# Performance work log

Measured on AMD Instinct MI355X. Metric: run time of the kernel, lower is better.

Reference implementation:

```python
import jax, jax.numpy as jnp
import numpy as np

B, Q, V, H = 8, 128, 512, 512


def setup_inputs() -> dict:
    key = jax.random.key(0)
    ks = jax.random.split(key, 6)
    s = 1.0 / np.sqrt(H)
    return {
        "query": jax.random.normal(ks[0], (B, Q, H), jnp.float32),
        "values": jax.random.normal(ks[1], (B, V, H), jnp.float32),
        "mask": jax.random.randint(ks[2], (B, V), 0, 2, jnp.int32),
        "Wq": jax.random.normal(ks[3], (H, H), jnp.float32) * s,
        "bq": jnp.zeros((H,), jnp.float32),
        "Wv": jax.random.normal(ks[4], (H, H), jnp.float32) * s,
        "bv": jnp.zeros((H,), jnp.float32),
        "wc": jax.random.normal(ks[5], (H, 1), jnp.float32) * s,
        "bc": jnp.zeros((1,), jnp.float32),
    }


def reference(query, values, mask, Wq, bq, Wv, bv, wc, bc):
    # Project once per token (Q*H and V*H GEMMs), then broadcast-add:
    # faithful to tanh(Lq(q)[:, :, None] + Lv(v)[:, None]) since Linear is
    # applied along the last dim and broadcasting commutes with it.
    qp = jnp.einsum('bqh,kh->bqk', query, Wq) + bq          # [B,Q,H]
    vp = jnp.einsum('bvh,kh->bvk', values, Wv) + bv          # [B,V,H]
    added = jnp.tanh(qp[:, :, None, :] + vp[:, None, :, :])  # [B,Q,V,H]
    scores = jnp.einsum('bqvh,ho->bqv', added, wc) + bc[0]   # [B,Q,V]
    neg_inf = jnp.array(-jnp.inf, scores.dtype)
    scores = jnp.where(mask[:, None, :] == 0, neg_inf, scores)
    weights = jax.nn.softmax(scores, axis=-1)                # [B,Q,V]
    context = jnp.einsum('bqv,bvh->bqh', weights, values)    # [B,Q,H]
    return (context, weights)
```

## Files before the change

kernel.cpp:

```cpp
#include <hip/hip_runtime.h>
#include <hip/hip_bf16.h>


#define C_SCALE 2.8853900817779268f

typedef __attribute__((ext_vector_type(8))) short short8;
typedef __attribute__((ext_vector_type(4))) float f32x4;

__device__ __forceinline__ float fexp2(float x) { return __builtin_amdgcn_exp2f(x); }
__device__ __forceinline__ float frcp(float x)  { return __builtin_amdgcn_rcpf(x); }

__device__ __forceinline__ void bf_split(float x, short& hi, short& lo) {
  unsigned u = __builtin_bit_cast(unsigned, x);
  unsigned r = u + 0x7fffu + ((u >> 16) & 1u);
  hi = (short)(r >> 16);
  float hf = __builtin_bit_cast(float, r & 0xffff0000u);
  lo = (short)(__builtin_bit_cast(unsigned, x - hf) >> 16);
}

__global__ __launch_bounds__(256) void proj_gemm_mfma(
    const float* __restrict__ query, const float* __restrict__ values,
    const float* __restrict__ Wq, const float* __restrict__ Wv,
    const float* __restrict__ bq, const float* __restrict__ bv,
    float* __restrict__ qp, float* __restrict__ vp)
{
  __shared__ short sAhi[64 * 72];
  __shared__ short sAlo[64 * 72];
  __shared__ short sWhi[64 * 72];
  __shared__ short sWlo[64 * 72];

  const int t    = threadIdx.x;
  const int lane = t & 63;
  const int w    = t >> 6;
  const int by   = blockIdx.y;
  const bool isQ = (by < 16);
  const float* A    = isQ ? query : values;
  const float* W    = isQ ? Wq : Wv;
  const float* bias = isQ ? bq : bv;
  float*       out  = isQ ? qp : vp;
  const int m0 = (isQ ? by : (by - 16)) << 6;
  const int n0 = blockIdx.x << 6;

  const int srow = t >> 2, scol = t & 3;
  const float* Ap = A + (size_t)(m0 + srow) * 512 + (scol << 2);
  const float* Wp = W + (size_t)(n0 + srow) * 512 + (scol << 2);

  const int mw = (w & 1) << 5, nw = (w >> 1) << 5;
  const int frow = lane & 15, fquad = lane >> 4;

  f32x4 acc[2][2] = {};
  float4 pfA[4], pfW[4];
#pragma unroll
  for (int p = 0; p < 4; ++p) {
    pfA[p] = *(const float4*)(Ap + (p << 4));
    pfW[p] = *(const float4*)(Wp + (p << 4));
  }

  for (int kc = 0; kc < 512; kc += 64) {
    __syncthreads();
#pragma unroll
    for (int p = 0; p < 4; ++p) {
      float av[4] = {pfA[p].x, pfA[p].y, pfA[p].z, pfA[p].w};
      float wv[4] = {pfW[p].x, pfW[p].y, pfW[p].z, pfW[p].w};
      short4 ah, al, wh, wl;
      short* ahp = (short*)&ah; short* alp = (short*)&al;
      short* whp = (short*)&wh; short* wlp = (short*)&wl;
#pragma unroll
      for (int k = 0; k < 4; ++k) {
        bf_split(av[k], ahp[k], alp[k]);
        bf_split(wv[k], whp[k], wlp[k]);
      }
      const int ofs = srow * 72 + ((p << 2) + scol) * 4;
      *(short4*)&sAhi[ofs] = ah; *(short4*)&sAlo[ofs] = al;
      *(short4*)&sWhi[ofs] = wh; *(short4*)&sWlo[ofs] = wl;
    }
    __syncthreads();
    if (kc + 64 < 512) {
#pragma unroll
      for (int p = 0; p < 4; ++p) {
        pfA[p] = *(const float4*)(Ap + kc + 64 + (p << 4));
        pfW[p] = *(const float4*)(Wp + kc + 64 + (p << 4));
      }
    }
#pragma unroll
    for (int kb = 0; kb < 2; ++kb) {
      const int ko = kb * 32 + fquad * 8;
      short8 ahi[2], alo[2], whi[2], wlo[2];
#pragma unroll
      for (int mt = 0; mt < 2; ++mt) {
        const int r = (mw + mt * 16 + frow) * 72 + ko;
        ahi[mt] = *(const short8*)&sAhi[r];
        alo[mt] = *(const short8*)&sAlo[r];
      }
#pragma unroll
      for (int nt = 0; nt < 2; ++nt) {
        const int r = (nw + nt * 16 + frow) * 72 + ko;
        whi[nt] = *(const short8*)&sWhi[r];
        wlo[nt] = *(const short8*)&sWlo[r];
      }
#pragma unroll
      for (int mt = 0; mt < 2; ++mt)
#pragma unroll
        for (int nt = 0; nt < 2; ++nt) {
          acc[mt][nt] = __builtin_amdgcn_mfma_f32_16x16x32_bf16(
              alo[mt], whi[nt], acc[mt][nt], 0, 0, 0);
          acc[mt][nt] = __builtin_amdgcn_mfma_f32_16x16x32_bf16(
              ahi[mt], wlo[nt], acc[mt][nt], 0, 0, 0);
          acc[mt][nt] = __builtin_amdgcn_mfma_f32_16x16x32_bf16(
              ahi[mt], whi[nt], acc[mt][nt], 0, 0, 0);
        }
    }
  }

#pragma unroll
  for (int nt = 0; nt < 2; ++nt) {
    const int n = n0 + nw + nt * 16 + frow;
    const float bn = bias[n];
#pragma unroll
    for (int mt = 0; mt < 2; ++mt) {
      float vreg[4] = {acc[mt][nt].x, acc[mt][nt].y, acc[mt][nt].z, acc[mt][nt].w};
#pragma unroll
      for (int r = 0; r < 4; ++r) {
        const int m = m0 + mw + mt * 16 + fquad * 4 + r;
        out[(size_t)m * 512 + n] = vreg[r] + bn;
      }
    }
  }
}

template<int NU>
__device__ __forceinline__ void score_chunk(
    const float* __restrict__ vpb, const float* __restrict__ qr0,
    const float* __restrict__ qr1, const float* __restrict__ wc,
    const int* idxs, float* wls0, float* wls1,
    int sbase, int i0, int g, int c4, int cnt, int lane)
{
  unsigned voff[NU];
  float a0[NU], a1[NU];
#pragma unroll
  for (int u = 0; u < NU; ++u) {
    const int s = (sbase + ((i0 + u) << 2) + g) & 511;
    voff[u] = ((unsigned)idxs[s] << 9) + (unsigned)c4;
    a0[u] = 0.f; a1[u] = 0.f;
  }
#pragma unroll
  for (int j = 0; j < 8; ++j) {
    const int hoff = (j << 6) + c4;
    const float4 q0v = *(const float4*)(qr0 + hoff);
    const float4 q1v = *(const float4*)(qr1 + hoff);
    const float4 wcv = *(const float4*)(wc + hoff);
    const unsigned jo = (unsigned)(j << 6);
    float4 vv[NU];
#pragma unroll
    for (int u = 0; u < NU; ++u)
      vv[u] = *(const float4*)(vpb + (voff[u] + jo));
    const float cq0[4] = {C_SCALE * q0v.x, C_SCALE * q0v.y,
                          C_SCALE * q0v.z, C_SCALE * q0v.w};
    const float dd[4]  = {fexp2(C_SCALE * (q1v.x - q0v.x)),
                          fexp2(C_SCALE * (q1v.y - q0v.y)),
                          fexp2(C_SCALE * (q1v.z - q0v.z)),
                          fexp2(C_SCALE * (q1v.w - q0v.w))};
    const float wc4[4] = {wcv.x, wcv.y, wcv.z, wcv.w};
#pragma unroll
    for (int u = 0; u < NU; ++u) {
      const float vq[4] = {vv[u].x, vv[u].y, vv[u].z, vv[u].w};
#pragma unroll
      for (int k = 0; k < 4; ++k) {
        float x0 = __builtin_fmaf(C_SCALE, vq[k], cq0[k]);
        float e0 = fexp2(x0);
        float e1 = e0 * dd[k];
        float d0 = e0 + 1.0f;
        float d1 = e1 + 1.0f;
        float P  = frcp(d0 * d1);
        a0[u] = __builtin_fmaf(wc4[k] * d1, P, a0[u]);
        a1[u] = __builtin_fmaf(wc4[k] * d0, P, a1[u]);
      }
    }
  }
#pragma unroll
  for (int u = 0; u < NU; ++u) {
    const int i = i0 + u;
    float s0 = a0[u], s1 = a1[u];
#pragma unroll
    for (int off = 1; off < 16; off <<= 1) {
      s0 += __shfl_xor(s0, off, 64);
      s1 += __shfl_xor(s1, off, 64);
    }
    const int s = sbase + (i << 2) + g;
    if ((lane & 15) == i && s < cnt) { wls0[s] = s0; wls1[s] = s1; }
  }
}

__global__ __launch_bounds__(512) void attn_fused(
    const float* __restrict__ qp, const float* __restrict__ vp,
    const float* __restrict__ values, const int* __restrict__ mask,
    const float* __restrict__ wc,
    float* __restrict__ out_ctx, float* __restrict__ out_w)
{
  __shared__ int   idxs[512];
  __shared__ float wls[2][512];
  __shared__ float wls2[512][2];
  __shared__ int   cnt8[8];

  const int t    = threadIdx.x;
  const int lane = t & 63;
  const int w    = t >> 6;
  const int b    = blockIdx.x & 7;
  const int qg   = blockIdx.x >> 3;
  const int rowbase = b * 128 + qg * 2;

  ((float*)wls)[t]        = 3.4e38f;
  ((float*)wls)[t + 512]  = 3.4e38f;
  ((float*)wls2)[t]       = 0.f;
  ((float*)wls2)[t + 512] = 0.f;
  idxs[t] = 0;
  if (t < 256) {
    float4 z = {0.f, 0.f, 0.f, 0.f};
    ((float4*)(out_w + (size_t)rowbase * 512))[t] = z;
  }
  const int mv = mask[b * 512 + t];
  const unsigned long long bal = __ballot(mv != 0);
  if (lane == 0) cnt8[w] = __popcll(bal);
  __syncthreads();
  int cnt = 0, offw = 0;
#pragma unroll
  for (int j = 0; j < 8; ++j) { if (j == w) offw = cnt; cnt += cnt8[j]; }
  if (mv) {
    int rank = __popcll(bal & ((1ull << lane) - 1ull));
    idxs[offw + rank] = t;
  }
  __syncthreads();

  const int NSTEP = (cnt + 31) >> 5;
  const int sbase = w * (NSTEP << 2);
  const int g  = lane >> 4;
  const int c4 = (lane & 15) << 2;

  const float* vpb = vp + (size_t)b * 512 * 512;
  const float* qr0 = qp + (size_t)rowbase * 512;
  const float* qr1 = qr0 + 512;

  int i0 = 0;
  for (; i0 + 4 <= NSTEP; i0 += 4)
    score_chunk<4>(vpb, qr0, qr1, wc, idxs, wls[0], wls[1],
                   sbase, i0, g, c4, cnt, lane);
  for (; i0 < NSTEP; ++i0)
    score_chunk<1>(vpb, qr0, qr1, wc, idxs, wls[0], wls[1],
                   sbase, i0, g, c4, cnt, lane);
  __syncthreads();

  {
    const int mq = (w >= 4) ? 1 : 0;
    const float* sc = wls[mq];
    float4 u0 = ((const float4*)sc)[lane * 2];
    float4 u1 = ((const float4*)sc)[lane * 2 + 1];
    float s8[8] = {u0.x, u0.y, u0.z, u0.w, u1.x, u1.y, u1.z, u1.w};
    float m = s8[0];
#pragma unroll
    for (int k = 1; k < 8; ++k) m = fminf(m, s8[k]);
#pragma unroll
    for (int off = 1; off < 64; off <<= 1) m = fminf(m, __shfl_xor(m, off, 64));
    float e[8], S = 0.f;
#pragma unroll
    for (int k = 0; k < 8; ++k) { e[k] = fexp2(C_SCALE * (m - s8[k])); S += e[k]; }
#pragma unroll
    for (int off = 1; off < 64; off <<= 1) S += __shfl_xor(S, off, 64);
    const float rinv = frcp(S);
    if (w == 0 || w == 4) {
      float* owq = out_w + (size_t)(rowbase + mq) * 512;
#pragma unroll
      for (int k = 0; k < 8; ++k) {
        const int s = lane * 8 + k;
        const float wgt = e[k] * rinv;
        wls2[s][mq] = wgt;
        if (s < cnt) owq[idxs[s]] = wgt;
      }
    }
  }
  __syncthreads();

  const int NC = (cnt + 3) >> 2;
  const unsigned hbase = (unsigned)(w * 64 + c4);
  const float* vb = values + (size_t)b * 512 * 512;
  float c0[4] = {0.f, 0.f, 0.f, 0.f}, c1[4] = {0.f, 0.f, 0.f, 0.f};
#pragma unroll 4
  for (int i = 0; i < NC; ++i) {
    const int s = (i << 2) + g;
    const unsigned ro = ((unsigned)idxs[s] << 9) + hbase;
    const float2 wg = *(const float2*)&wls2[s][0];
    const float4 v4 = *(const float4*)(vb + ro);
    float vv[4] = {v4.x, v4.y, v4.z, v4.w};
#pragma unroll
    for (int k = 0; k < 4; ++k) {
      c0[k] = __builtin_fmaf(wg.x, vv[k], c0[k]);
      c1[k] = __builtin_fmaf(wg.y, vv[k], c1[k]);
    }
  }
#pragma unroll
  for (int k = 0; k < 4; ++k) {
    c0[k] += __shfl_xor(c0[k], 16, 64); c0[k] += __shfl_xor(c0[k], 32, 64);
    c1[k] += __shfl_xor(c1[k], 16, 64); c1[k] += __shfl_xor(c1[k], 32, 64);
  }
  if (lane < 16) {
    float4 o0 = {c0[0], c0[1], c0[2], c0[3]};
    float4 o1 = {c1[0], c1[1], c1[2], c1[3]};
    *(float4*)(out_ctx + (size_t)rowbase * 512 + w * 64 + lane * 4)       = o0;
    *(float4*)(out_ctx + (size_t)(rowbase + 1) * 512 + w * 64 + lane * 4) = o1;
  }
}

extern "C" void kernel_launch(void* const* d_in, const int* in_sizes, int n_in,
                              void* d_out, int out_size, void* d_ws, size_t ws_size,
                              hipStream_t stream) {
  const float* query  = (const float*)d_in[0];
  const float* values = (const float*)d_in[1];
  const int*   mask   = (const int*)d_in[2];
  const float* Wq     = (const float*)d_in[3];
  const float* bq     = (const float*)d_in[4];
  const float* Wv     = (const float*)d_in[5];
  const float* bv     = (const float*)d_in[6];
  const float* wc     = (const float*)d_in[7];

  float* out = (float*)d_out;
  float* qp  = (float*)d_ws;
  float* vp  = qp + (size_t)1024 * 512;

  proj_gemm_mfma<<<dim3(8, 80), 256, 0, stream>>>(query, values, Wq, Wv, bq, bv, qp, vp);
  attn_fused<<<512, 512, 0, stream>>>(qp, vp, values, mask, wc,
                                      out, out + (size_t)8 * 128 * 512);
}
```

Before: 145.8 us.

## Split fused attention into score and finish kernels with 4-way key split

Splits the fused attention kernel into a score kernel launched on a 512x4 grid of 256-thread blocks, each handling a quarter of the unmasked keys. Scores are staged in the weights output buffer instead of shared memory, and a second kernel runs softmax, scatters the weights and computes the context. The goal is more concurrent blocks and better latency hiding for the dominant tanh-score work. In exchange it adds a kernel launch, recomputes the mask compaction in each block, and round-trips the scores through global memory.

```diff
diff --git a/kernel.cpp b/kernel.cpp
--- a/kernel.cpp
+++ b/kernel.cpp
@@ -129,31 +129,30 @@
 }
 
 template<int NU>
-__device__ __forceinline__ void score_chunk(
+__device__ __forceinline__ void score_chunkA(
     const float* __restrict__ vpb, const float* __restrict__ qr0,
-    const float* __restrict__ qr1, const float* __restrict__ wc,
-    const int* idxs, float* wls0, float* wls1,
-    int sbase, int i0, int g, int c4, int cnt, int lane)
+    const float* __restrict__ wc, const int* idxs, float* __restrict__ ow0,
+    int s00, int i0, int hi, int c4, int lane)
 {
+  int su[NU];
   unsigned voff[NU];
   float a0[NU], a1[NU];
 #pragma unroll
   for (int u = 0; u < NU; ++u) {
-    const int s = (sbase + ((i0 + u) << 2) + g) & 511;
-    voff[u] = ((unsigned)idxs[s] << 9) + (unsigned)c4;
+    su[u] = s00 + ((i0 + u) << 4);
+    voff[u] = ((unsigned)idxs[su[u] & 511] << 9) + (unsigned)c4;
     a0[u] = 0.f; a1[u] = 0.f;
   }
 #pragma unroll
   for (int j = 0; j < 8; ++j) {
     const int hoff = (j << 6) + c4;
+    float4 vv[NU];
+#pragma unroll
+    for (int u = 0; u < NU; ++u)
+      vv[u] = *(const float4*)(vpb + voff[u] + (unsigned)(j << 6));
     const float4 q0v = *(const float4*)(qr0 + hoff);
-    const float4 q1v = *(const float4*)(qr1 + hoff);
+    const float4 q1v = *(const float4*)(qr0 + 512 + hoff);
     const float4 wcv = *(const float4*)(wc + hoff);
-    const unsigned jo = (unsigned)(j << 6);
-    float4 vv[NU];
-#pragma unroll
-    for (int u = 0; u < NU; ++u)
-      vv[u] = *(const float4*)(vpb + (voff[u] + jo));
     const float cq0[4] = {C_SCALE * q0v.x, C_SCALE * q0v.y,
                           C_SCALE * q0v.z, C_SCALE * q0v.w};
     const float dd[4]  = {fexp2(C_SCALE * (q1v.x - q0v.x)),
@@ -179,28 +178,26 @@
   }
 #pragma unroll
   for (int u = 0; u < NU; ++u) {
-    const int i = i0 + u;
     float s0 = a0[u], s1 = a1[u];
 #pragma unroll
     for (int off = 1; off < 16; off <<= 1) {
       s0 += __shfl_xor(s0, off, 64);
       s1 += __shfl_xor(s1, off, 64);
     }
-    const int s = sbase + (i << 2) + g;
-    if ((lane & 15) == i && s < cnt) { wls0[s] = s0; wls1[s] = s1; }
-  }
-}
-
-__global__ __launch_bounds__(512) void attn_fused(
+    if (su[u] < hi && (lane & 15) == (i0 + u)) {
+      ow0[su[u]]       = s0;
+      ow0[512 + su[u]] = s1;
+    }
+  }
+}
+
+__global__ __launch_bounds__(256, 8) void attn_score(
     const float* __restrict__ qp, const float* __restrict__ vp,
-    const float* __restrict__ values, const int* __restrict__ mask,
-    const float* __restrict__ wc,
-    float* __restrict__ out_ctx, float* __restrict__ out_w)
+    const int* __restrict__ mask, const float* __restrict__ wc,
+    float* __restrict__ out_w)
 {
-  __shared__ int   idxs[512];
-  __shared__ float wls[2][512];
-  __shared__ float wls2[512][2];
-  __shared__ int   cnt8[8];
+  __shared__ int idxs[512];
+  __shared__ int cnt8[8];
 
   const int t    = threadIdx.x;
   const int lane = t & 63;
@@ -209,15 +206,61 @@
   const int qg   = blockIdx.x >> 3;
   const int rowbase = b * 128 + qg * 2;
 
-  ((float*)wls)[t]        = 3.4e38f;
-  ((float*)wls)[t + 512]  = 3.4e38f;
+  idxs[t] = 0; idxs[t + 256] = 0;
+  const int mv0 = mask[b * 512 + t];
+  const int mv1 = mask[b * 512 + 256 + t];
+  const unsigned long long bal0 = __ballot(mv0 != 0);
+  const unsigned long long bal1 = __ballot(mv1 != 0);
+  if (lane == 0) { cnt8[w] = __popcll(bal0); cnt8[w + 4] = __popcll(bal1); }
+  __syncthreads();
+  int cnt = 0, off0 = 0, off4 = 0;
+#pragma unroll
+  for (int j = 0; j < 8; ++j) {
+    if (j == w)     off0 = cnt;
+    if (j == w + 4) off4 = cnt;
+    cnt += cnt8[j];
+  }
+  if (mv0) idxs[off0 + __popcll(bal0 & ((1ull << lane) - 1ull))] = t;
+  if (mv1) idxs[off4 + __popcll(bal1 & ((1ull << lane) - 1ull))] = t + 256;
+  __syncthreads();
+
+  const int c  = blockIdx.y;
+  const int lo = (cnt * c) >> 2;
+  const int hi = (cnt * (c + 1)) >> 2;
+  const int NI = (hi - lo + 15) >> 4;
+  const int g  = lane >> 4;
+  const int c4 = (lane & 15) << 2;
+  const int s00 = lo + (w << 2) + g;
+
+  const float* vpb = vp + (size_t)b * 512 * 512;
+  const float* qr0 = qp + (size_t)rowbase * 512;
+  float* ow0 = out_w + (size_t)rowbase * 512;
+
+  int i0 = 0;
+  for (; i0 + 2 <= NI; i0 += 2)
+    score_chunkA<2>(vpb, qr0, wc, idxs, ow0, s00, i0, hi, c4, lane);
+  for (; i0 < NI; ++i0)
+    score_chunkA<1>(vpb, qr0, wc, idxs, ow0, s00, i0, hi, c4, lane);
+}
+
+__global__ __launch_bounds__(512) void attn_finish(
+    const float* __restrict__ values, const int* __restrict__ mask,
+    float* __restrict__ out_ctx, float* __restrict__ out_w)
+{
+  __shared__ int   idxs[512];
+  __shared__ float wls2[512][2];
+  __shared__ int   cnt8[8];
+
+  const int t    = threadIdx.x;
+  const int lane = t & 63;
+  const int w    = t >> 6;
+  const int b    = blockIdx.x & 7;
+  const int qg   = blockIdx.x >> 3;
+  const int rowbase = b * 128 + qg * 2;
+
   ((float*)wls2)[t]       = 0.f;
   ((float*)wls2)[t + 512] = 0.f;
   idxs[t] = 0;
-  if (t < 256) {
-    float4 z = {0.f, 0.f, 0.f, 0.f};
-    ((float4*)(out_w + (size_t)rowbase * 512))[t] = z;
-  }
   const int mv = mask[b * 512 + t];
   const unsigned long long bal = __ballot(mv != 0);
   if (lane == 0) cnt8[w] = __popcll(bal);
@@ -225,36 +268,22 @@
   int cnt = 0, offw = 0;
 #pragma unroll
   for (int j = 0; j < 8; ++j) { if (j == w) offw = cnt; cnt += cnt8[j]; }
+  int iinv = -1;
   if (mv) {
-    int rank = __popcll(bal & ((1ull << lane) - 1ull));
-    idxs[offw + rank] = t;
-  }
-  __syncthreads();
-
-  const int NSTEP = (cnt + 31) >> 5;
-  const int sbase = w * (NSTEP << 2);
-  const int g  = lane >> 4;
-  const int c4 = (lane & 15) << 2;
-
-  const float* vpb = vp + (size_t)b * 512 * 512;
-  const float* qr0 = qp + (size_t)rowbase * 512;
-  const float* qr1 = qr0 + 512;
-
-  int i0 = 0;
-  for (; i0 + 4 <= NSTEP; i0 += 4)
-    score_chunk<4>(vpb, qr0, qr1, wc, idxs, wls[0], wls[1],
-                   sbase, i0, g, c4, cnt, lane);
-  for (; i0 < NSTEP; ++i0)
-    score_chunk<1>(vpb, qr0, qr1, wc, idxs, wls[0], wls[1],
-                   sbase, i0, g, c4, cnt, lane);
+    iinv = offw + __popcll(bal & ((1ull << lane) - 1ull));
+    idxs[iinv] = t;
+  }
   __syncthreads();
 
   {
     const int mq = (w >= 4) ? 1 : 0;
-    const float* sc = wls[mq];
-    float4 u0 = ((const float4*)sc)[lane * 2];
-    float4 u1 = ((const float4*)sc)[lane * 2 + 1];
+    const float* srow = out_w + (size_t)(rowbase + mq) * 512;
+    float4 u0 = ((const float4*)srow)[lane * 2];
+    float4 u1 = ((const float4*)srow)[lane * 2 + 1];
     float s8[8] = {u0.x, u0.y, u0.z, u0.w, u1.x, u1.y, u1.z, u1.w};
+#pragma unroll
+    for (int k = 0; k < 8; ++k)
+      if (lane * 8 + k >= cnt) s8[k] = 3.4e38f;
     float m = s8[0];
 #pragma unroll
     for (int k = 1; k < 8; ++k) m = fminf(m, s8[k]);
@@ -267,19 +296,25 @@
     for (int off = 1; off < 64; off <<= 1) S += __shfl_xor(S, off, 64);
     const float rinv = frcp(S);
     if (w == 0 || w == 4) {
-      float* owq = out_w + (size_t)(rowbase + mq) * 512;
 #pragma unroll
       for (int k = 0; k < 8; ++k) {
         const int s = lane * 8 + k;
-        const float wgt = e[k] * rinv;
-        wls2[s][mq] = wgt;
-        if (s < cnt) owq[idxs[s]] = wgt;
-      }
-    }
-  }
-  __syncthreads();
+        if (s < cnt) wls2[s][mq] = e[k] * rinv;
+      }
+    }
+  }
+  __syncthreads();
+
+  {
+    float w0 = 0.f, w1 = 0.f;
+    if (iinv >= 0) { w0 = wls2[iinv][0]; w1 = wls2[iinv][1]; }
+    out_w[(size_t)rowbase * 512 + t]       = w0;
+    out_w[(size_t)(rowbase + 1) * 512 + t] = w1;
+  }
 
   const int NC = (cnt + 3) >> 2;
+  const int g  = lane >> 4;
+  const int c4 = (lane & 15) << 2;
   const unsigned hbase = (unsigned)(w * 64 + c4);
   const float* vb = values + (size_t)b * 512 * 512;
   float c0[4] = {0.f, 0.f, 0.f, 0.f}, c1[4] = {0.f, 0.f, 0.f, 0.f};
@@ -321,11 +356,12 @@
   const float* bv     = (const float*)d_in[6];
   const float* wc     = (const float*)d_in[7];
 
-  float* out = (float*)d_out;
-  float* qp  = (float*)d_ws;
-  float* vp  = qp + (size_t)1024 * 512;
+  float* out   = (float*)d_out;
+  float* out_w = out + (size_t)8 * 128 * 512;
+  float* qp    = (float*)d_ws;
+  float* vp    = qp + (size_t)1024 * 512;
 
   proj_gemm_mfma<<<dim3(8, 80), 256, 0, stream>>>(query, values, Wq, Wv, bq, bv, qp, vp);
-  attn_fused<<<512, 512, 0, stream>>>(qp, vp, values, mask, wc,
-                                      out, out + (size_t)8 * 128 * 512);
-}
+  attn_score<<<dim3(512, 4), 256, 0, stream>>>(qp, vp, mask, wc, out_w);
+  attn_finish<<<512, 512, 0, stream>>>(values, mask, out, out_w);
+}
```

After: 264.9 us. 81.7% more time.
